# Kernel optimization log

Hardware: AMD Instinct MI355X
Metric: run time of the kernel (lower is better)

Reference implementation:

```python
import jax, jax.numpy as jnp
import numpy as np

B, T = 16, 2048
D_EMB, D_CND2, H_RNN, H_FC, N_OUT = 256, 640, 896, 1024, 1024


def setup_inputs() -> dict:
    key = jax.random.key(0)
    ks = jax.random.split(key, 12)
    s = 0.02
    return {
        "reference_sample": jax.random.randint(ks[0], (B, T), 0, N_OUT),
        "i_cnd_series": jax.random.normal(ks[1], (B, T, D_CND2), dtype=jnp.float32),
        "emb": jax.random.normal(ks[2], (N_OUT, D_EMB), dtype=jnp.float32) * s,
        "W_ih": jax.random.normal(ks[3], (3 * H_RNN, D_EMB + D_CND2), dtype=jnp.float32) * s,
        "b_ih": jnp.zeros((3 * H_RNN,), jnp.float32),
        "W_hh": jax.random.normal(ks[4], (3 * H_RNN, H_RNN), dtype=jnp.float32) * s,
        "b_hh": jnp.zeros((3 * H_RNN,), jnp.float32),
        "fc1_w": jax.random.normal(ks[5], (H_FC, H_RNN), dtype=jnp.float32) * s,
        "fc1_b": jnp.zeros((H_FC,), jnp.float32),
        "fc2_w": jax.random.normal(ks[6], (N_OUT, H_FC), dtype=jnp.float32) * s,
        "fc2_b": jnp.zeros((N_OUT,), jnp.float32),
    }


def _gru(x, W_ih, b_ih, W_hh, b_hh):
    # x: [B, T, D_in] -> hidden states [B, T, H] (PyTorch GRU gate order r, z, n)
    Bn = x.shape[0]
    gx = jnp.einsum("btd,gd->btg", x, W_ih) + b_ih  # precompute input gates [B,T,3H]
    gx = jnp.transpose(gx, (1, 0, 2))  # [T,B,3H]

    def step(h, gxt):
        gh = h @ W_hh.T + b_hh
        rx, zx, nx = jnp.split(gxt, 3, axis=-1)
        rh, zh, nh = jnp.split(gh, 3, axis=-1)
        r = jax.nn.sigmoid(rx + rh)
        z = jax.nn.sigmoid(zx + zh)
        n = jnp.tanh(nx + r * nh)
        h_new = (1.0 - z) * n + z * h
        return h_new, h_new

    h0 = jnp.zeros((Bn, W_hh.shape[1]), x.dtype)
    _, hs = jax.lax.scan(step, h0, gx)
    return jnp.transpose(hs, (1, 0, 2))  # [B,T,H]


def reference(reference_sample, i_cnd_series, emb, W_ih, b_ih, W_hh, b_hh,
              fc1_w, fc1_b, fc2_w, fc2_b):
    x_emb = emb[reference_sample]                      # [B,T,D_EMB]
    x = jnp.concatenate([x_emb, i_cnd_series], axis=2)  # [B,T,D_EMB+2*cnd]
    o_rnn = _gru(x, W_ih, b_ih, W_hh, b_hh)            # [B,T,H_RNN]
    h = jax.nn.relu(jnp.einsum("bth,fh->btf", o_rnn, fc1_w) + fc1_b)
    return jnp.einsum("btf,of->bto", h, fc2_w) + fc2_b  # [B,T,N_OUT]
```

## Files before the change

kernel.cpp:

```cpp
#include <hip/hip_runtime.h>
#include <hip/hip_bf16.h>

typedef __bf16 bf16;
typedef __bf16 bf16x8 __attribute__((ext_vector_type(8)));
typedef float  floatx4 __attribute__((ext_vector_type(4)));

#define NWG 56

static constexpr size_t CT_OFF  = 0;
static constexpr size_t HB_OFF  = 256;
static constexpr size_t WBF_OFF = 256 + 114688;
static constexpr size_t GX_OFF  = WBF_OFF + 13565952;
static constexpr size_t HSX_OFF = GX_OFF + 176160768;

static constexpr size_t W_IH_E = 2688 * 896;
static constexpr size_t W_HH_E = 2688 * 896;
static constexpr size_t W_F1_E = 1024 * 896;

__device__ __forceinline__ float sigm(float x)      { return 1.f / (1.f + __expf(-x)); }
__device__ __forceinline__ float fast_tanh(float x) { return 2.f / (1.f + __expf(-2.f * x)) - 1.f; }

__global__ __launch_bounds__(256) void k_cvt(const float* __restrict__ src,
                                             bf16* __restrict__ dst)
{
    const int s = blockIdx.x * 256 + threadIdx.x;
    const float4 a = ((const float4*)src)[s * 2 + 0];
    const float4 b = ((const float4*)src)[s * 2 + 1];
    bf16x8 v;
    v[0] = (bf16)a.x; v[1] = (bf16)a.y; v[2] = (bf16)a.z; v[3] = (bf16)a.w;
    v[4] = (bf16)b.x; v[5] = (bf16)b.y; v[6] = (bf16)b.z; v[7] = (bf16)b.w;
    ((bf16x8*)dst)[s] = v;
}

__global__ __launch_bounds__(256) void k_embed(const int* __restrict__ samp,
                                               const float* __restrict__ cnd,
                                               const float* __restrict__ emb,
                                               bf16* __restrict__ x)
{
    const int s = blockIdx.x * 256 + threadIdx.x;
    const int r = s / 112;
    const int c = s % 112;
    const float* src;
    if (c < 32) src = emb + samp[r] * 256 + c * 8;
    else        src = cnd + (long)r * 640 + (c - 32) * 8;
    const float4 a = ((const float4*)src)[0];
    const float4 b = ((const float4*)src)[1];
    bf16x8 v;
    v[0] = (bf16)a.x; v[1] = (bf16)a.y; v[2] = (bf16)a.z; v[3] = (bf16)a.w;
    v[4] = (bf16)b.x; v[5] = (bf16)b.y; v[6] = (bf16)b.z; v[7] = (bf16)b.w;
    *(bf16x8*)(x + (long)r * 896 + c * 8) = v;
}

template <int RELU, int GXMODE, int OUTF32>
__global__ __launch_bounds__(256, 2) void gemm_bt(const bf16* __restrict__ A,
                                                  const bf16* __restrict__ Bw,
                                                  const float* __restrict__ bias,
                                                  void* __restrict__ Cv,
                                                  int M, int N, int K)
{
    __shared__ bf16 As[128 * 40];
    __shared__ bf16 Bs[128 * 40];

    const int tid  = threadIdx.x;
    const int lane = tid & 63;
    const int wv   = tid >> 6;
    const int wm   = wv >> 1;
    const int wn   = wv & 1;
    const int n16  = lane & 15;
    const int quad = lane >> 4;
    const int tm   = blockIdx.y * 128;
    const int tn   = blockIdx.x * 128;

    floatx4 acc[4][4] = {};

    const int s0 = tid, s1 = tid + 256;
    const int r0 = s0 >> 2, c0 = s0 & 3;
    const int r1 = s1 >> 2, c1 = s1 & 3;

    const int KT = K >> 5;
    for (int kt = 0; kt < KT; ++kt) {
        const int k0 = kt * 32;
        bf16x8 a0 = *(const bf16x8*)(A  + (long)(tm + r0) * K + k0 + c0 * 8);
        bf16x8 a1 = *(const bf16x8*)(A  + (long)(tm + r1) * K + k0 + c1 * 8);
        bf16x8 b0 = *(const bf16x8*)(Bw + (long)(tn + r0) * K + k0 + c0 * 8);
        bf16x8 b1 = *(const bf16x8*)(Bw + (long)(tn + r1) * K + k0 + c1 * 8);
        __syncthreads();
        *(bf16x8*)(As + r0 * 40 + c0 * 8) = a0;
        *(bf16x8*)(As + r1 * 40 + c1 * 8) = a1;
        *(bf16x8*)(Bs + r0 * 40 + c0 * 8) = b0;
        *(bf16x8*)(Bs + r1 * 40 + c1 * 8) = b1;
        __syncthreads();

        bf16x8 af[4], bfj[4];
#pragma unroll
        for (int i = 0; i < 4; ++i)
            af[i] = *(const bf16x8*)(As + (wm * 64 + i * 16 + n16) * 40 + quad * 8);
#pragma unroll
        for (int j = 0; j < 4; ++j)
            bfj[j] = *(const bf16x8*)(Bs + (wn * 64 + j * 16 + n16) * 40 + quad * 8);
#pragma unroll
        for (int i = 0; i < 4; ++i)
#pragma unroll
            for (int j = 0; j < 4; ++j)
                acc[i][j] = __builtin_amdgcn_mfma_f32_16x16x32_bf16(af[i], bfj[j], acc[i][j], 0, 0, 0);
    }

#pragma unroll
    for (int j = 0; j < 4; ++j) {
        const int c = tn + wn * 64 + j * 16 + n16;
        const float bv = bias[c];
#pragma unroll
        for (int i = 0; i < 4; ++i) {
            const int rbase = tm + wm * 64 + i * 16 + quad * 4;
#pragma unroll
            for (int rr = 0; rr < 4; ++rr) {
                float v = acc[i][j][rr] + bv;
                if (RELU) v = fmaxf(v, 0.f);
                const int r = rbase + rr;
                long oidx;
                if (GXMODE) { const int tt = r & 2047, bb = r >> 11; oidx = (long)(tt * 16 + bb) * N + c; }
                else        { oidx = (long)r * N + c; }
                if (OUTF32) ((float*)Cv)[oidx] = v;
                else        ((bf16*)Cv)[oidx]  = (bf16)v;
            }
        }
    }
}

__global__ __launch_bounds__(192, 1) void gru_scan(const bf16* __restrict__ Whh,
                                                   const float* __restrict__ bhh,
                                                   const bf16* __restrict__ gx,
                                                   bf16* __restrict__ hs,
                                                   float* __restrict__ hbuf,
                                                   unsigned int* __restrict__ ctr)
{
    __shared__ bf16  hst[16 * 904];
    __shared__ float gacc[3][16][16];
    __shared__ float bhs[3][16];

    const int tid  = threadIdx.x;
    const int wv   = tid >> 6;
    const int lane = tid & 63;
    const int n16  = lane & 15;
    const int quad = lane >> 4;
    const int col0 = blockIdx.x * 16;

    bf16x8 wf[28];
    {
        const bf16* wrow = Whh + (long)(wv * 896 + col0 + n16) * 896;
#pragma unroll
        for (int kt = 0; kt < 28; ++kt)
            wf[kt] = *(const bf16x8*)(wrow + kt * 32 + quad * 8);
    }
    if (tid < 48) bhs[tid / 16][tid % 16] = bhh[(tid / 16) * 896 + col0 + (tid % 16)];
    __syncthreads();

    for (int t = 0; t < 2048; ++t) {
        const int p = t & 1;
        const float* hsrc = hbuf + p * (16 * 896);
        float*       hdst = hbuf + (1 - p) * (16 * 896);

        float gxv[6];
        const int b  = tid >> 3;
        const int c2 = (tid & 7) * 2;
        if (tid < 128) {
            const bf16* g0 = gx + (long)(t * 16 + b) * 2688 + col0 + c2;
#pragma unroll
            for (int g = 0; g < 3; ++g) {
                gxv[g * 2 + 0] = (float)g0[g * 896 + 0];
                gxv[g * 2 + 1] = (float)g0[g * 896 + 1];
            }
        }

        {
            float4 ta[9], tb[9];
#pragma unroll
            for (int it = 0; it < 9; ++it) {
                const int s = tid + it * 192;
                const float* sp = hsrc + (s / 112) * 896 + (s % 112) * 8;
                ta[it] = ((const float4*)sp)[0];
                tb[it] = ((const float4*)sp)[1];
            }
            float4 tc, td;
            if (tid < 64) {
                const int s = tid + 1728;
                const float* sp = hsrc + (s / 112) * 896 + (s % 112) * 8;
                tc = ((const float4*)sp)[0];
                td = ((const float4*)sp)[1];
            }
#pragma unroll
            for (int it = 0; it < 9; ++it) {
                const int s = tid + it * 192;
                bf16x8 v;
                v[0] = (bf16)ta[it].x; v[1] = (bf16)ta[it].y; v[2] = (bf16)ta[it].z; v[3] = (bf16)ta[it].w;
                v[4] = (bf16)tb[it].x; v[5] = (bf16)tb[it].y; v[6] = (bf16)tb[it].z; v[7] = (bf16)tb[it].w;
                *(bf16x8*)(hst + (s / 112) * 904 + (s % 112) * 8) = v;
            }
            if (tid < 64) {
                const int s = tid + 1728;
                bf16x8 v;
                v[0] = (bf16)tc.x; v[1] = (bf16)tc.y; v[2] = (bf16)tc.z; v[3] = (bf16)tc.w;
                v[4] = (bf16)td.x; v[5] = (bf16)td.y; v[6] = (bf16)td.z; v[7] = (bf16)td.w;
                *(bf16x8*)(hst + (s / 112) * 904 + (s % 112) * 8) = v;
            }
        }
        __syncthreads();

        floatx4 acc = {0.f, 0.f, 0.f, 0.f};
#pragma unroll
        for (int kt = 0; kt < 28; ++kt) {
            bf16x8 af = *(const bf16x8*)(hst + n16 * 904 + kt * 32 + quad * 8);
            acc = __builtin_amdgcn_mfma_f32_16x16x32_bf16(af, wf[kt], acc, 0, 0, 0);
        }
#pragma unroll
        for (int r = 0; r < 4; ++r) gacc[wv][quad * 4 + r][n16] = acc[r];
        __syncthreads();

        if (tid < 128) {
#pragma unroll
            for (int u = 0; u < 2; ++u) {
                const int c = c2 + u;
                const float ghr = gacc[0][b][c] + bhs[0][c];
                const float ghz = gacc[1][b][c] + bhs[1][c];
                const float ghn = gacc[2][b][c] + bhs[2][c];
                const float rg = sigm(gxv[0 + u] + ghr);
                const float zg = sigm(gxv[2 + u] + ghz);
                const float ng = fast_tanh(gxv[4 + u] + rg * ghn);
                const float hold = hsrc[b * 896 + col0 + c];
                const float hnew = (1.f - zg) * ng + zg * hold;
                hdst[b * 896 + col0 + c] = hnew;
                hs[((long)b * 2048 + t) * 896 + col0 + c] = (bf16)hnew;
            }
        }

        __syncthreads();
        if (tid == 0) {
            __threadfence();
            __hip_atomic_fetch_add(ctr, 1u, __ATOMIC_RELAXED, __HIP_MEMORY_SCOPE_AGENT);
            const unsigned tgt = (unsigned)NWG * (unsigned)(t + 1);
            while (__hip_atomic_load(ctr, __ATOMIC_RELAXED, __HIP_MEMORY_SCOPE_AGENT) < tgt)
                __builtin_amdgcn_s_sleep(2);
            __threadfence();
        }
        __syncthreads();
    }
}

extern "C" void kernel_launch(void* const* d_in, const int* in_sizes, int n_in,
                              void* d_out, int out_size, void* d_ws, size_t ws_size,
                              hipStream_t stream)
{
    const int*   samp = (const int*)d_in[0];
    const float* cnd  = (const float*)d_in[1];
    const float* emb  = (const float*)d_in[2];
    const float* Wih  = (const float*)d_in[3];
    const float* bih  = (const float*)d_in[4];
    const float* Whh  = (const float*)d_in[5];
    const float* bhh  = (const float*)d_in[6];
    const float* fc1w = (const float*)d_in[7];
    const float* fc1b = (const float*)d_in[8];
    const float* fc2w = (const float*)d_in[9];
    const float* fc2b = (const float*)d_in[10];

    char* ws = (char*)d_ws;
    unsigned int* ctr = (unsigned int*)(ws + CT_OFF);
    float* hbuf = (float*)(ws + HB_OFF);
    bf16*  wbf  = (bf16*)(ws + WBF_OFF);
    bf16*  gx   = (bf16*)(ws + GX_OFF);
    bf16*  hs   = (bf16*)(ws + HSX_OFF);
    bf16*  x    = (bf16*)(ws + HSX_OFF);
    bf16*  h1   = (bf16*)(ws + GX_OFF);

    bf16* wih_bf = wbf;
    bf16* whh_bf = wbf + W_IH_E;
    bf16* fc1_bf = whh_bf + W_HH_E;
    bf16* fc2_bf = fc1_bf + W_F1_E;

    (void)hipMemsetAsync(ctr, 0, 256, stream);
    (void)hipMemsetAsync(hbuf, 0, 2 * 16 * 896 * 4, stream);

    k_cvt<<<1176, 256, 0, stream>>>(Wih,  wih_bf);
    k_cvt<<<1176, 256, 0, stream>>>(Whh,  whh_bf);
    k_cvt<<< 448, 256, 0, stream>>>(fc1w, fc1_bf);
    k_cvt<<< 512, 256, 0, stream>>>(fc2w, fc2_bf);

    k_embed<<<14336, 256, 0, stream>>>(samp, cnd, emb, x);
    gemm_bt<0, 1, 0><<<dim3(21, 256), 256, 0, stream>>>(x, wih_bf, bih, gx, 32768, 2688, 896);
    gru_scan<<<NWG, 192, 0, stream>>>(whh_bf, bhh, gx, hs, hbuf, ctr);
    gemm_bt<1, 0, 0><<<dim3(8, 256), 256, 0, stream>>>(hs, fc1_bf, fc1b, h1, 32768, 1024, 896);
    gemm_bt<0, 0, 1><<<dim3(8, 256), 256, 0, stream>>>(h1, fc2_bf, fc2b, d_out, 32768, 1024, 1024);
}
```

Baseline: 13.85 ms.

## Replace GRU scan global atomic barrier with per-workgroup flags and bf16 hidden exchange

The single shared atomic counter barrier is replaced by per-workgroup step flags, each padded to its own 128-byte line. Each workgroup publishes its flag with a release store and polls all 56 flags in one wavefront, so it no longer contends on one counter. The exchanged hidden state becomes bf16 in a tile-blocked layout with the fp32 state kept in registers, which halves the cross-workgroup traffic. The input-gate load for the next step is prefetched after the flag store. Risks are the extra spinning and the reduced precision of the exchanged h, although the MFMA already consumed it as bf16.

```diff
diff --git a/kernel.cpp b/kernel.cpp
--- a/kernel.cpp
+++ b/kernel.cpp
@@ -2,14 +2,15 @@
 #include <hip/hip_bf16.h>
 
 typedef __bf16 bf16;
+typedef __bf16 bf16x2 __attribute__((ext_vector_type(2)));
 typedef __bf16 bf16x8 __attribute__((ext_vector_type(8)));
 typedef float  floatx4 __attribute__((ext_vector_type(4)));
 
 #define NWG 56
 
-static constexpr size_t CT_OFF  = 0;
-static constexpr size_t HB_OFF  = 256;
-static constexpr size_t WBF_OFF = 256 + 114688;
+static constexpr size_t FL_OFF  = 0;
+static constexpr size_t HB_OFF  = 8192;
+static constexpr size_t WBF_OFF = 65536;
 static constexpr size_t GX_OFF  = WBF_OFF + 13565952;
 static constexpr size_t HSX_OFF = GX_OFF + 176160768;
 
@@ -131,8 +132,8 @@
                                                    const float* __restrict__ bhh,
                                                    const bf16* __restrict__ gx,
                                                    bf16* __restrict__ hs,
-                                                   float* __restrict__ hbuf,
-                                                   unsigned int* __restrict__ ctr)
+                                                   bf16* __restrict__ hbuf,
+                                                   unsigned int* __restrict__ flags)
 {
     __shared__ bf16  hst[16 * 904];
     __shared__ float gacc[3][16][16];
@@ -143,7 +144,8 @@
     const int lane = tid & 63;
     const int n16  = lane & 15;
     const int quad = lane >> 4;
-    const int col0 = blockIdx.x * 16;
+    const int wg   = blockIdx.x;
+    const int col0 = wg * 16;
 
     bf16x8 wf[28];
     {
@@ -153,55 +155,57 @@
             wf[kt] = *(const bf16x8*)(wrow + kt * 32 + quad * 8);
     }
     if (tid < 48) bhs[tid / 16][tid % 16] = bhh[(tid / 16) * 896 + col0 + (tid % 16)];
+
+    const int u0 = tid - 64;
+    const int b  = u0 >> 3;
+    const int c2 = (u0 & 7) * 2;
+    float hl0 = 0.f, hl1 = 0.f;
+    float gxv[6];
+    if (tid >= 64) {
+        const bf16* g0 = gx + (long)(0 * 16 + b) * 2688 + col0 + c2;
+#pragma unroll
+        for (int g = 0; g < 3; ++g) {
+            gxv[g * 2 + 0] = (float)g0[g * 896 + 0];
+            gxv[g * 2 + 1] = (float)g0[g * 896 + 1];
+        }
+    }
     __syncthreads();
 
     for (int t = 0; t < 2048; ++t) {
-        const int p = t & 1;
-        const float* hsrc = hbuf + p * (16 * 896);
-        float*       hdst = hbuf + (1 - p) * (16 * 896);
-
-        float gxv[6];
-        const int b  = tid >> 3;
-        const int c2 = (tid & 7) * 2;
-        if (tid < 128) {
-            const bf16* g0 = gx + (long)(t * 16 + b) * 2688 + col0 + c2;
-#pragma unroll
-            for (int g = 0; g < 3; ++g) {
-                gxv[g * 2 + 0] = (float)g0[g * 896 + 0];
-                gxv[g * 2 + 1] = (float)g0[g * 896 + 1];
-            }
-        }
+        const bf16* hb_cur  = hbuf + (t & 1) * (56 * 256);
+        bf16*       hb_next = hbuf + ((t + 1) & 1) * (56 * 256);
+
+        if (tid < 64) {
+            if (t > 0) {
+                for (;;) {
+                    unsigned f = (lane < NWG)
+                        ? __hip_atomic_load(flags + lane * 32, __ATOMIC_RELAXED, __HIP_MEMORY_SCOPE_AGENT)
+                        : 0xFFFFFFFFu;
+                    if (__all(f >= (unsigned)t)) break;
+                    __builtin_amdgcn_s_sleep(1);
+                }
+            }
+            __threadfence();
+        }
+        __syncthreads();
 
         {
-            float4 ta[9], tb[9];
+            bf16x8 seg[9];
+#pragma unroll
+            for (int it = 0; it < 9; ++it)
+                seg[it] = *(const bf16x8*)(hb_cur + (tid + it * 192) * 8);
+            bf16x8 segl;
+            if (tid < 64) segl = *(const bf16x8*)(hb_cur + (1728 + tid) * 8);
 #pragma unroll
             for (int it = 0; it < 9; ++it) {
                 const int s = tid + it * 192;
-                const float* sp = hsrc + (s / 112) * 896 + (s % 112) * 8;
-                ta[it] = ((const float4*)sp)[0];
-                tb[it] = ((const float4*)sp)[1];
-            }
-            float4 tc, td;
+                const int ct = s >> 5, rem = s & 31, bb = rem >> 1, hf = rem & 1;
+                *(bf16x8*)(hst + bb * 904 + ct * 16 + hf * 8) = seg[it];
+            }
             if (tid < 64) {
-                const int s = tid + 1728;
-                const float* sp = hsrc + (s / 112) * 896 + (s % 112) * 8;
-                tc = ((const float4*)sp)[0];
-                td = ((const float4*)sp)[1];
-            }
-#pragma unroll
-            for (int it = 0; it < 9; ++it) {
-                const int s = tid + it * 192;
-                bf16x8 v;
-                v[0] = (bf16)ta[it].x; v[1] = (bf16)ta[it].y; v[2] = (bf16)ta[it].z; v[3] = (bf16)ta[it].w;
-                v[4] = (bf16)tb[it].x; v[5] = (bf16)tb[it].y; v[6] = (bf16)tb[it].z; v[7] = (bf16)tb[it].w;
-                *(bf16x8*)(hst + (s / 112) * 904 + (s % 112) * 8) = v;
-            }
-            if (tid < 64) {
-                const int s = tid + 1728;
-                bf16x8 v;
-                v[0] = (bf16)tc.x; v[1] = (bf16)tc.y; v[2] = (bf16)tc.z; v[3] = (bf16)tc.w;
-                v[4] = (bf16)td.x; v[5] = (bf16)td.y; v[6] = (bf16)td.z; v[7] = (bf16)td.w;
-                *(bf16x8*)(hst + (s / 112) * 904 + (s % 112) * 8) = v;
+                const int s = 1728 + tid;
+                const int ct = s >> 5, rem = s & 31, bb = rem >> 1, hf = rem & 1;
+                *(bf16x8*)(hst + bb * 904 + ct * 16 + hf * 8) = segl;
             }
         }
         __syncthreads();
@@ -216,7 +220,9 @@
         for (int r = 0; r < 4; ++r) gacc[wv][quad * 4 + r][n16] = acc[r];
         __syncthreads();
 
-        if (tid < 128) {
+        if (tid >= 64) {
+            float hn[2];
+            const float hold[2] = { hl0, hl1 };
 #pragma unroll
             for (int u = 0; u < 2; ++u) {
                 const int c = c2 + u;
@@ -226,23 +232,30 @@
                 const float rg = sigm(gxv[0 + u] + ghr);
                 const float zg = sigm(gxv[2 + u] + ghz);
                 const float ng = fast_tanh(gxv[4 + u] + rg * ghn);
-                const float hold = hsrc[b * 896 + col0 + c];
-                const float hnew = (1.f - zg) * ng + zg * hold;
-                hdst[b * 896 + col0 + c] = hnew;
-                hs[((long)b * 2048 + t) * 896 + col0 + c] = (bf16)hnew;
-            }
-        }
-
-        __syncthreads();
+                hn[u] = (1.f - zg) * ng + zg * hold[u];
+            }
+            hl0 = hn[0]; hl1 = hn[1];
+            bf16x2 hv; hv[0] = (bf16)hn[0]; hv[1] = (bf16)hn[1];
+            *(bf16x2*)(hb_next + wg * 256 + b * 16 + c2) = hv;
+            *(bf16x2*)(hs + ((long)b * 2048 + t) * 896 + col0 + c2) = hv;
+        }
+        __syncthreads();
+
         if (tid == 0) {
             __threadfence();
-            __hip_atomic_fetch_add(ctr, 1u, __ATOMIC_RELAXED, __HIP_MEMORY_SCOPE_AGENT);
-            const unsigned tgt = (unsigned)NWG * (unsigned)(t + 1);
-            while (__hip_atomic_load(ctr, __ATOMIC_RELAXED, __HIP_MEMORY_SCOPE_AGENT) < tgt)
-                __builtin_amdgcn_s_sleep(2);
-            __threadfence();
-        }
-        __syncthreads();
+            __hip_atomic_store(flags + wg * 32, (unsigned)(t + 1),
+                               __ATOMIC_RELEASE, __HIP_MEMORY_SCOPE_AGENT);
+        }
+
+        if (tid >= 64) {
+            const int tn_ = (t + 1 < 2048) ? (t + 1) : 2047;
+            const bf16* g0 = gx + (long)(tn_ * 16 + b) * 2688 + col0 + c2;
+#pragma unroll
+            for (int g = 0; g < 3; ++g) {
+                gxv[g * 2 + 0] = (float)g0[g * 896 + 0];
+                gxv[g * 2 + 1] = (float)g0[g * 896 + 1];
+            }
+        }
     }
 }
 
@@ -263,21 +276,21 @@
     const float* fc2b = (const float*)d_in[10];
 
     char* ws = (char*)d_ws;
-    unsigned int* ctr = (unsigned int*)(ws + CT_OFF);
-    float* hbuf = (float*)(ws + HB_OFF);
-    bf16*  wbf  = (bf16*)(ws + WBF_OFF);
-    bf16*  gx   = (bf16*)(ws + GX_OFF);
-    bf16*  hs   = (bf16*)(ws + HSX_OFF);
-    bf16*  x    = (bf16*)(ws + HSX_OFF);
-    bf16*  h1   = (bf16*)(ws + GX_OFF);
+    unsigned int* flags = (unsigned int*)(ws + FL_OFF);
+    bf16* hbuf = (bf16*)(ws + HB_OFF);
+    bf16* wbf  = (bf16*)(ws + WBF_OFF);
+    bf16* gx   = (bf16*)(ws + GX_OFF);
+    bf16* hs   = (bf16*)(ws + HSX_OFF);
+    bf16* x    = (bf16*)(ws + HSX_OFF);
+    bf16* h1   = (bf16*)(ws + GX_OFF);
 
     bf16* wih_bf = wbf;
     bf16* whh_bf = wbf + W_IH_E;
     bf16* fc1_bf = whh_bf + W_HH_E;
     bf16* fc2_bf = fc1_bf + W_F1_E;
 
-    (void)hipMemsetAsync(ctr, 0, 256, stream);
-    (void)hipMemsetAsync(hbuf, 0, 2 * 16 * 896 * 4, stream);
+    (void)hipMemsetAsync(flags, 0, 8192, stream);
+    (void)hipMemsetAsync(hbuf, 0, 57344, stream);
 
     k_cvt<<<1176, 256, 0, stream>>>(Wih,  wih_bf);
     k_cvt<<<1176, 256, 0, stream>>>(Whh,  whh_bf);
@@ -286,7 +299,7 @@
 
     k_embed<<<14336, 256, 0, stream>>>(samp, cnd, emb, x);
     gemm_bt<0, 1, 0><<<dim3(21, 256), 256, 0, stream>>>(x, wih_bf, bih, gx, 32768, 2688, 896);
-    gru_scan<<<NWG, 192, 0, stream>>>(whh_bf, bhh, gx, hs, hbuf, ctr);
+    gru_scan<<<NWG, 192, 0, stream>>>(whh_bf, bhh, gx, hs, hbuf, flags);
     gemm_bt<1, 0, 0><<<dim3(8, 256), 256, 0, stream>>>(hs, fc1_bf, fc1b, h1, 32768, 1024, 896);
     gemm_bt<0, 0, 1><<<dim3(8, 256), 256, 0, stream>>>(h1, fc2_bf, fc2b, d_out, 32768, 1024, 1024);
 }
```

New measurement: 11.89 ms. 1.16x faster.
